# Performance work log

Measured on AMD Instinct MI355X. Metric: run time of the kernel, lower is better.

The kernel has to match this reference:

```python
import jax, jax.numpy as jnp
import numpy as np

B, T, D = 16, 2048, 256

def setup_inputs() -> dict:
    key = jax.random.key(0)
    k1, k2, k3 = jax.random.split(key, 3)
    q = jax.random.normal(k1, (B, T, D), dtype=jnp.float32)
    a = jax.random.normal(k2, (B, T, D), dtype=jnp.float32)
    # original uses 'uniform' init; scale ~ small
    U = jax.random.uniform(k3, (D, D), dtype=jnp.float32, minval=-0.05, maxval=0.05)
    return {"q": q, "a": a, "U": U}

def reference(q, a, U):
    # G[b,i,j] = tanh( (q[b,i,:] @ U) . a[b,j,:] )
    qU = jnp.einsum('btd,de->bte', q, U)                 # [B,Tq,D]
    G = jnp.tanh(jnp.einsum('btd,bsd->bts', qU, a))      # [B,Tq,Ta]
    g_q = jax.nn.softmax(jnp.max(G, axis=-1), axis=1)    # [B,Tq]
    g_a = jax.nn.softmax(jnp.max(G, axis=1), axis=1)     # [B,Ta]
    q_out = jnp.einsum('btd,bt->bd', q, g_q)             # [B,D]
    a_out = jnp.einsum('bsd,bs->bd', a, g_a)             # [B,D]
    return (q_out, a_out)
```

## Files before the change

### kernel.cpp

```cpp
#include <hip/hip_runtime.h>
#include <stdint.h>

typedef __attribute__((ext_vector_type(8))) short s8v;
typedef __attribute__((ext_vector_type(4))) float f4v;

__device__ __forceinline__ unsigned short f2bf(float f) {
  unsigned u = __float_as_uint(f);
  u = u + 0x7FFFu + ((u >> 16) & 1u);
  return (unsigned short)(u >> 16);
}
__device__ __forceinline__ unsigned encf(float f) {
  unsigned i = __float_as_uint(f);
  return (i & 0x80000000u) ? ~i : (i | 0x80000000u);
}
__device__ __forceinline__ float decf(unsigned u) {
  unsigned i = (u & 0x80000000u) ? (u & 0x7FFFFFFFu) : ~u;
  return __uint_as_float(i);
}
__device__ __forceinline__ void gload_lds16(const unsigned short* g, unsigned short* l) {
  __builtin_amdgcn_global_load_lds((const __attribute__((address_space(1))) void*)g,
                                   (__attribute__((address_space(3))) void*)l, 16, 0, 0);
}

__global__ void convert_kernel(const float4* __restrict__ q, const float4* __restrict__ a,
                               const float* __restrict__ U,
                               ushort4* __restrict__ qb, ushort4* __restrict__ ab,
                               unsigned short* __restrict__ Ut,
                               unsigned* __restrict__ rcmax) {
  const int bx = blockIdx.x;
  if (bx < 8192) {
    const int i = bx * 256 + threadIdx.x;
    float4 v = q[i];
    qb[i] = make_ushort4(f2bf(v.x), f2bf(v.y), f2bf(v.z), f2bf(v.w));
    float4 w = a[i];
    ab[i] = make_ushort4(f2bf(w.x), f2bf(w.y), f2bf(w.z), f2bf(w.w));
  } else if (bx < 8256) {
    const int idx = (bx - 8192) * 256 + threadIdx.x;
    const int n  = idx >> 6;
    const int k4 = (idx & 63) * 4;
    ushort4 o;
    o.x = f2bf(U[(k4 + 0) * 256 + n]);
    o.y = f2bf(U[(k4 + 1) * 256 + n]);
    o.z = f2bf(U[(k4 + 2) * 256 + n]);
    o.w = f2bf(U[(k4 + 3) * 256 + n]);
    *(ushort4*)&Ut[n * 256 + k4] = o;
  } else {
    const int idx = (bx - 8256) * 256 + threadIdx.x;
    *(uint4*)&rcmax[idx * 4] = make_uint4(0u, 0u, 0u, 0u);
  }
}

template<int MODE>
__global__ __launch_bounds__(256, 4)
void gemm_bt(const unsigned short* __restrict__ A,
             const unsigned short* __restrict__ Bm,
             long strideA, long strideB,
             unsigned short* __restrict__ C,
             unsigned* __restrict__ rowmax,
             unsigned* __restrict__ colmax,
             float* __restrict__ outz) {
  constexpr int AROWS = 128;
  constexpr int BROWS = 128;
  constexpr int RPI = 32;

  __shared__ unsigned short As[AROWS * 64];
  __shared__ unsigned short Bs[BROWS * 64];
  __shared__ unsigned rowLds[AROWS];
  __shared__ unsigned colLds[BROWS];

  const int tid = threadIdx.x;
  int tm, tn, b;
  if (MODE == 1) { b = blockIdx.x; tn = blockIdx.y; tm = blockIdx.z; }
  else           { tm = blockIdx.x; tn = blockIdx.y; b = blockIdx.z; }
  const unsigned short* Ab = A + (long)b * strideA + (long)tm * AROWS * 256;
  const unsigned short* Bb = Bm + (long)b * strideB + (long)tn * BROWS * 256;

  const int lane = tid & 63;
  const int m16  = lane & 15;
  const int quad = lane >> 4;
  const int wave = tid >> 6;
  const int wm   = wave >> 1, wn = wave & 1;
  const int srow = tid >> 3;
  const int scol = (((tid & 7) ^ (srow & 7))) * 8;

  if (MODE == 1) {
    if (tid < AROWS) rowLds[tid] = 0u;
    if (tid < BROWS) colLds[tid] = 0u;
    if (tn == 0 && tm == 0) {
      outz[b * 256 + tid] = 0.f;
      outz[4096 + b * 256 + tid] = 0.f;
    }
  }

  f4v acc[4][4] = {};

  for (int kt = 0; kt < 4; ++kt) {
    const int k0 = kt * 64;
    __syncthreads();
    #pragma unroll
    for (int i = 0; i < AROWS / RPI; ++i) {
      const int r = i * RPI + srow;
      gload_lds16(Ab + (long)r * 256 + k0 + scol, &As[i * RPI * 64 + tid * 8]);
    }
    #pragma unroll
    for (int i = 0; i < BROWS / RPI; ++i) {
      const int r = i * RPI + srow;
      gload_lds16(Bb + (long)r * 256 + k0 + scol, &Bs[i * RPI * 64 + tid * 8]);
    }
    __syncthreads();
    #pragma unroll
    for (int kk = 0; kk < 2; ++kk) {
      const int cs = ((kk * 4 + quad) ^ (m16 & 7)) * 8;
      s8v af[4], bfv[4];
      #pragma unroll
      for (int i = 0; i < 4; ++i)
        af[i] = *(const s8v*)&As[(wm * 64 + i * 16 + m16) * 64 + cs];
      #pragma unroll
      for (int j = 0; j < 4; ++j)
        bfv[j] = *(const s8v*)&Bs[(wn * 64 + j * 16 + m16) * 64 + cs];
      #pragma unroll
      for (int i = 0; i < 4; ++i)
        #pragma unroll
        for (int j = 0; j < 4; ++j)
          acc[i][j] = __builtin_amdgcn_mfma_f32_16x16x32_bf16(af[i], bfv[j], acc[i][j], 0, 0, 0);
    }
  }

  if (MODE == 0) {
    #pragma unroll
    for (int i = 0; i < 4; ++i)
      #pragma unroll
      for (int r = 0; r < 4; ++r) {
        const long row = (long)tm * AROWS + wm * 64 + i * 16 + quad * 4 + r;
        #pragma unroll
        for (int j = 0; j < 4; ++j) {
          const int col = tn * BROWS + wn * 64 + j * 16 + m16;
          C[row * 256 + col] = f2bf(acc[i][j][r]);
        }
      }
  } else {
    #pragma unroll
    for (int i = 0; i < 4; ++i)
      #pragma unroll
      for (int r = 0; r < 4; ++r) {
        float v = fmaxf(fmaxf(acc[i][0][r], acc[i][1][r]), fmaxf(acc[i][2][r], acc[i][3][r]));
        #pragma unroll
        for (int d2 = 1; d2 < 16; d2 <<= 1) v = fmaxf(v, __shfl_xor(v, d2));
        if (m16 == 0) atomicMax(&rowLds[wm * 64 + i * 16 + quad * 4 + r], encf(v));
      }
    #pragma unroll
    for (int j = 0; j < 4; ++j) {
      float v = -3.4e38f;
      #pragma unroll
      for (int i = 0; i < 4; ++i)
        #pragma unroll
        for (int r = 0; r < 4; ++r) v = fmaxf(v, acc[i][j][r]);
      v = fmaxf(v, __shfl_xor(v, 16));
      v = fmaxf(v, __shfl_xor(v, 32));
      if (quad == 0) atomicMax(&colLds[wn * 64 + j * 16 + m16], encf(v));
    }
    __syncthreads();
    if (tid < AROWS)
      atomicMax(&rowmax[(long)b * 2048 + tm * AROWS + tid], rowLds[tid]);
    if (tid < BROWS)
      atomicMax(&colmax[(long)b * 2048 + tn * BROWS + tid], colLds[tid]);
  }
}

__global__ void wsum_kernel(const uint4* __restrict__ qb, const uint4* __restrict__ ab,
                            const unsigned* __restrict__ rowmax, const unsigned* __restrict__ colmax,
                            float* __restrict__ out) {
  const int tid = threadIdx.x;
  const int chunk = blockIdx.x;
  const int b = blockIdx.y;
  const int z = blockIdx.z;
  const unsigned* e = z ? colmax : rowmax;
  const uint4* src = z ? ab : qb;

  __shared__ float sm[4];
  __shared__ float ss[4];
  __shared__ float wLds[128];
  __shared__ float red[256 * 8];

  float x[8];
  float m = -3.4e38f;
  #pragma unroll
  for (int j = 0; j < 8; ++j) {
    x[j] = tanhf(decf(e[b * 2048 + j * 256 + tid]));
    m = fmaxf(m, x[j]);
  }
  #pragma unroll
  for (int d2 = 1; d2 < 64; d2 <<= 1) m = fmaxf(m, __shfl_xor(m, d2));
  if ((tid & 63) == 0) sm[tid >> 6] = m;
  __syncthreads();
  m = fmaxf(fmaxf(sm[0], sm[1]), fmaxf(sm[2], sm[3]));
  float s = 0.f;
  #pragma unroll
  for (int j = 0; j < 8; ++j) s += expf(x[j] - m);
  #pragma unroll
  for (int d2 = 1; d2 < 64; d2 <<= 1) s += __shfl_xor(s, d2);
  if ((tid & 63) == 0) ss[tid >> 6] = s;
  __syncthreads();
  const float inv = 1.f / (ss[0] + ss[1] + ss[2] + ss[3]);

  if (tid < 128) {
    float xv = tanhf(decf(e[b * 2048 + chunk * 128 + tid]));
    wLds[tid] = expf(xv - m) * inv;
  }
  __syncthreads();

  const int dg = tid & 31;
  const int rg = tid >> 5;
  float acc[8] = {};
  const long rowbase = (long)b * 2048 + chunk * 128;
  for (int t = rg; t < 128; t += 8) {
    const float wgt = wLds[t];
    uint4 v = src[(rowbase + t) * 32 + dg];
    acc[0] += wgt * __uint_as_float(v.x << 16);
    acc[1] += wgt * __uint_as_float(v.x & 0xFFFF0000u);
    acc[2] += wgt * __uint_as_float(v.y << 16);
    acc[3] += wgt * __uint_as_float(v.y & 0xFFFF0000u);
    acc[4] += wgt * __uint_as_float(v.z << 16);
    acc[5] += wgt * __uint_as_float(v.z & 0xFFFF0000u);
    acc[6] += wgt * __uint_as_float(v.w << 16);
    acc[7] += wgt * __uint_as_float(v.w & 0xFFFF0000u);
  }
  #pragma unroll
  for (int k = 0; k < 8; ++k) red[tid * 8 + k] = acc[k];
  __syncthreads();
  if (tid < 32) {
    #pragma unroll
    for (int k = 0; k < 8; ++k) {
      float v = 0.f;
      #pragma unroll
      for (int g = 0; g < 8; ++g) v += red[((g << 5) | tid) * 8 + k];
      atomicAdd(&out[z * 4096 + b * 256 + tid * 8 + k], v);
    }
  }
}

extern "C" void kernel_launch(void* const* d_in, const int* in_sizes, int n_in,
                              void* d_out, int out_size, void* d_ws, size_t ws_size,
                              hipStream_t stream) {
  const float* q = (const float*)d_in[0];
  const float* a = (const float*)d_in[1];
  const float* U = (const float*)d_in[2];
  float* out = (float*)d_out;

  char* w = (char*)d_ws;
  unsigned short* qb = (unsigned short*)w;
  unsigned short* ab = (unsigned short*)(w + (16ull << 20));
  unsigned short* qU = (unsigned short*)(w + (32ull << 20));
  unsigned short* Ut = (unsigned short*)(w + (48ull << 20));
  unsigned* rmax = (unsigned*)(w + (48ull << 20) + (128ull << 10));
  unsigned* cmax = rmax + 32768;

  convert_kernel<<<8192 + 64 + 64, 256, 0, stream>>>((const float4*)q, (const float4*)a, U,
                                                     (ushort4*)qb, (ushort4*)ab, Ut, rmax);

  gemm_bt<0><<<dim3(256, 2, 1), 256, 0, stream>>>(qb, Ut, 0, 0, qU,
                                                  nullptr, nullptr, nullptr);

  gemm_bt<1><<<dim3(16, 16, 16), 256, 0, stream>>>(qU, ab, 2048 * 256, 2048 * 256,
                                                   nullptr, rmax, cmax, out);

  wsum_kernel<<<dim3(16, 16, 2), 256, 0, stream>>>((const uint4*)qb, (const uint4*)ab,
                                                   rmax, cmax, out);
}
```

Baseline: 173.3 us.

## Fuse q bf16 conversion into qU GEMM load and read fp32 q in wsum

```diff
diff --git a/kernel.cpp b/kernel.cpp
--- a/kernel.cpp
+++ b/kernel.cpp
@@ -9,6 +9,9 @@
   u = u + 0x7FFFu + ((u >> 16) & 1u);
   return (unsigned short)(u >> 16);
 }
+__device__ __forceinline__ unsigned f2bf2(float lo, float hi) {
+  return (unsigned)f2bf(lo) | ((unsigned)f2bf(hi) << 16);
+}
 __device__ __forceinline__ unsigned encf(float f) {
   unsigned i = __float_as_uint(f);
   return (i & 0x80000000u) ? ~i : (i | 0x80000000u);
@@ -22,16 +25,12 @@
                                    (__attribute__((address_space(3))) void*)l, 16, 0, 0);
 }
 
-__global__ void convert_kernel(const float4* __restrict__ q, const float4* __restrict__ a,
-                               const float* __restrict__ U,
-                               ushort4* __restrict__ qb, ushort4* __restrict__ ab,
-                               unsigned short* __restrict__ Ut,
-                               unsigned* __restrict__ rcmax) {
+__global__ void convert_kernel(const float4* __restrict__ a, const float* __restrict__ U,
+                               ushort4* __restrict__ ab, unsigned short* __restrict__ Ut,
+                               unsigned* __restrict__ rcmax, float* __restrict__ out) {
   const int bx = blockIdx.x;
   if (bx < 8192) {
     const int i = bx * 256 + threadIdx.x;
-    float4 v = q[i];
-    qb[i] = make_ushort4(f2bf(v.x), f2bf(v.y), f2bf(v.z), f2bf(v.w));
     float4 w = a[i];
     ab[i] = make_ushort4(f2bf(w.x), f2bf(w.y), f2bf(w.z), f2bf(w.w));
   } else if (bx < 8256) {
@@ -44,21 +43,21 @@
     o.z = f2bf(U[(k4 + 2) * 256 + n]);
     o.w = f2bf(U[(k4 + 3) * 256 + n]);
     *(ushort4*)&Ut[n * 256 + k4] = o;
-  } else {
+  } else if (bx < 8320) {
     const int idx = (bx - 8256) * 256 + threadIdx.x;
     *(uint4*)&rcmax[idx * 4] = make_uint4(0u, 0u, 0u, 0u);
-  }
-}
-
-template<int MODE>
-__global__ __launch_bounds__(256, 4)
-void gemm_bt(const unsigned short* __restrict__ A,
-             const unsigned short* __restrict__ Bm,
-             long strideA, long strideB,
-             unsigned short* __restrict__ C,
-             unsigned* __restrict__ rowmax,
-             unsigned* __restrict__ colmax,
-             float* __restrict__ outz) {
+  } else {
+    out[(bx - 8320) * 256 + threadIdx.x] = 0.f;
+  }
+}
+
+template<int MODE, int AF32>
+__global__ void gemm_bt(const void* __restrict__ Av,
+                        const unsigned short* __restrict__ Bm,
+                        long strideA, long strideB,
+                        unsigned short* __restrict__ C,
+                        unsigned* __restrict__ rowmax,
+                        unsigned* __restrict__ colmax) {
   constexpr int AROWS = 128;
   constexpr int BROWS = 128;
   constexpr int RPI = 32;
@@ -72,7 +71,9 @@
   int tm, tn, b;
   if (MODE == 1) { b = blockIdx.x; tn = blockIdx.y; tm = blockIdx.z; }
   else           { tm = blockIdx.x; tn = blockIdx.y; b = blockIdx.z; }
-  const unsigned short* Ab = A + (long)b * strideA + (long)tm * AROWS * 256;
+  const long Aoff = (long)b * strideA + (long)tm * AROWS * 256;
+  const unsigned short* Au = (const unsigned short*)Av + Aoff;
+  const float* Af = (const float*)Av + Aoff;
   const unsigned short* Bb = Bm + (long)b * strideB + (long)tn * BROWS * 256;
 
   const int lane = tid & 63;
@@ -86,10 +87,6 @@
   if (MODE == 1) {
     if (tid < AROWS) rowLds[tid] = 0u;
     if (tid < BROWS) colLds[tid] = 0u;
-    if (tn == 0 && tm == 0) {
-      outz[b * 256 + tid] = 0.f;
-      outz[4096 + b * 256 + tid] = 0.f;
-    }
   }
 
   f4v acc[4][4] = {};
@@ -100,7 +97,16 @@
     #pragma unroll
     for (int i = 0; i < AROWS / RPI; ++i) {
       const int r = i * RPI + srow;
-      gload_lds16(Ab + (long)r * 256 + k0 + scol, &As[i * RPI * 64 + tid * 8]);
+      if constexpr (AF32) {
+        const float4* p = (const float4*)(Af + (long)r * 256 + k0 + scol);
+        float4 f0 = p[0], f1 = p[1];
+        uint4 wv;
+        wv.x = f2bf2(f0.x, f0.y); wv.y = f2bf2(f0.z, f0.w);
+        wv.z = f2bf2(f1.x, f1.y); wv.w = f2bf2(f1.z, f1.w);
+        *(uint4*)&As[i * RPI * 64 + tid * 8] = wv;
+      } else {
+        gload_lds16(Au + (long)r * 256 + k0 + scol, &As[i * RPI * 64 + tid * 8]);
+      }
     }
     #pragma unroll
     for (int i = 0; i < BROWS / RPI; ++i) {
@@ -160,14 +166,15 @@
       if (quad == 0) atomicMax(&colLds[wn * 64 + j * 16 + m16], encf(v));
     }
     __syncthreads();
-    if (tid < AROWS)
+    if (tid < AROWS) {
       atomicMax(&rowmax[(long)b * 2048 + tm * AROWS + tid], rowLds[tid]);
-    if (tid < BROWS)
-      atomicMax(&colmax[(long)b * 2048 + tn * BROWS + tid], colLds[tid]);
-  }
-}
-
-__global__ void wsum_kernel(const uint4* __restrict__ qb, const uint4* __restrict__ ab,
+    } else if (tid < AROWS + BROWS) {
+      atomicMax(&colmax[(long)b * 2048 + tn * BROWS + (tid - AROWS)], colLds[tid - AROWS]);
+    }
+  }
+}
+
+__global__ void wsum_kernel(const float4* __restrict__ qf, const uint4* __restrict__ ab,
                             const unsigned* __restrict__ rowmax, const unsigned* __restrict__ colmax,
                             float* __restrict__ out) {
   const int tid = threadIdx.x;
@@ -175,7 +182,6 @@
   const int b = blockIdx.y;
   const int z = blockIdx.z;
   const unsigned* e = z ? colmax : rowmax;
-  const uint4* src = z ? ab : qb;
 
   __shared__ float sm[4];
   __shared__ float ss[4];
@@ -213,17 +219,27 @@
   const int rg = tid >> 5;
   float acc[8] = {};
   const long rowbase = (long)b * 2048 + chunk * 128;
-  for (int t = rg; t < 128; t += 8) {
-    const float wgt = wLds[t];
-    uint4 v = src[(rowbase + t) * 32 + dg];
-    acc[0] += wgt * __uint_as_float(v.x << 16);
-    acc[1] += wgt * __uint_as_float(v.x & 0xFFFF0000u);
-    acc[2] += wgt * __uint_as_float(v.y << 16);
-    acc[3] += wgt * __uint_as_float(v.y & 0xFFFF0000u);
-    acc[4] += wgt * __uint_as_float(v.z << 16);
-    acc[5] += wgt * __uint_as_float(v.z & 0xFFFF0000u);
-    acc[6] += wgt * __uint_as_float(v.w << 16);
-    acc[7] += wgt * __uint_as_float(v.w & 0xFFFF0000u);
+  if (z == 0) {
+    for (int t = rg; t < 128; t += 8) {
+      const float wgt = wLds[t];
+      float4 u = qf[(rowbase + t) * 64 + dg * 2];
+      float4 v = qf[(rowbase + t) * 64 + dg * 2 + 1];
+      acc[0] += wgt * u.x; acc[1] += wgt * u.y; acc[2] += wgt * u.z; acc[3] += wgt * u.w;
+      acc[4] += wgt * v.x; acc[5] += wgt * v.y; acc[6] += wgt * v.z; acc[7] += wgt * v.w;
+    }
+  } else {
+    for (int t = rg; t < 128; t += 8) {
+      const float wgt = wLds[t];
+      uint4 v = ab[(rowbase + t) * 32 + dg];
+      acc[0] += wgt * __uint_as_float(v.x << 16);
+      acc[1] += wgt * __uint_as_float(v.x & 0xFFFF0000u);
+      acc[2] += wgt * __uint_as_float(v.y << 16);
+      acc[3] += wgt * __uint_as_float(v.y & 0xFFFF0000u);
+      acc[4] += wgt * __uint_as_float(v.z << 16);
+      acc[5] += wgt * __uint_as_float(v.z & 0xFFFF0000u);
+      acc[6] += wgt * __uint_as_float(v.w << 16);
+      acc[7] += wgt * __uint_as_float(v.w & 0xFFFF0000u);
+    }
   }
   #pragma unroll
   for (int k = 0; k < 8; ++k) red[tid * 8 + k] = acc[k];
@@ -248,22 +264,21 @@
   float* out = (float*)d_out;
 
   char* w = (char*)d_ws;
-  unsigned short* qb = (unsigned short*)w;
-  unsigned short* ab = (unsigned short*)(w + (16ull << 20));
-  unsigned short* qU = (unsigned short*)(w + (32ull << 20));
-  unsigned short* Ut = (unsigned short*)(w + (48ull << 20));
-  unsigned* rmax = (unsigned*)(w + (48ull << 20) + (128ull << 10));
+  unsigned short* ab = (unsigned short*)w;
+  unsigned short* qU = (unsigned short*)(w + (16ull << 20));
+  unsigned short* Ut = (unsigned short*)(w + (32ull << 20));
+  unsigned* rmax = (unsigned*)(w + (32ull << 20) + (128ull << 10));
   unsigned* cmax = rmax + 32768;
 
-  convert_kernel<<<8192 + 64 + 64, 256, 0, stream>>>((const float4*)q, (const float4*)a, U,
-                                                     (ushort4*)qb, (ushort4*)ab, Ut, rmax);
-
-  gemm_bt<0><<<dim3(256, 2, 1), 256, 0, stream>>>(qb, Ut, 0, 0, qU,
-                                                  nullptr, nullptr, nullptr);
-
-  gemm_bt<1><<<dim3(16, 16, 16), 256, 0, stream>>>(qU, ab, 2048 * 256, 2048 * 256,
-                                                   nullptr, rmax, cmax, out);
-
-  wsum_kernel<<<dim3(16, 16, 2), 256, 0, stream>>>((const uint4*)qb, (const uint4*)ab,
+  convert_kernel<<<8352, 256, 0, stream>>>((const float4*)a, U, (ushort4*)ab, Ut, rmax, out);
+
+  gemm_bt<0, 1><<<dim3(256, 2, 1), 256, 0, stream>>>((const void*)q, Ut, 0, 0, qU,
+                                                     nullptr, nullptr);
+
+  gemm_bt<1, 0><<<dim3(16, 16, 16), 256, 0, stream>>>((const void*)qU, ab,
+                                                      2048 * 256, 2048 * 256,
+                                                      nullptr, rmax, cmax);
+
+  wsum_kernel<<<dim3(16, 16, 2), 256, 0, stream>>>((const float4*)q, (const uint4*)ab,
                                                    rmax, cmax, out);
 }
```

After: 178.4 us. +2.9%, slower.
